# Performance work log

Measured on AMD Instinct MI355X. Metric: run time of the kernel, lower is better.

The kernel has to match this reference:

```python
import jax, jax.numpy as jnp
import numpy as np

B, W, N = 128, 128, 64
HID = 150  # lstm_hid_dim == recon_hid_dim
L = 2      # layer_numb


def _edges_fc(n):
    # for j in range(n) for i in range(n) if i != j -> row0 = i (src), row1 = j (dst)
    a = np.arange(n)
    src = np.concatenate([np.delete(a, j) for j in range(n)])
    dst = np.repeat(a, n - 1)
    return np.stack([src, dst]).astype(np.int32)


def _edges_tc(w):
    # for j in range(w) for i in range(j) -> row0 = i (src), row1 = j (dst)
    src = np.concatenate([np.arange(j) for j in range(1, w)])
    dst = np.repeat(np.arange(w), np.arange(w))
    return np.stack([src, dst]).astype(np.int32)


def _batch_edges(e, b, n):
    # tile per-graph edges b times with node offsets (block-diagonal batched graph)
    off = (jnp.arange(b) * n).astype(e.dtype)
    return (e[:, None, :] + off[None, :, None]).reshape(2, -1)


def _gat_conv(x, edge_index, w, a_src, a_dst, b):
    # PyG GATConv, heads=1: h = x W^T; e_ij = LeakyReLU(a_src.h_j + a_dst.h_i); softmax over dst
    m = x.shape[0]
    loop = jnp.arange(m, dtype=edge_index.dtype)
    src = jnp.concatenate([edge_index[0], loop])
    dst = jnp.concatenate([edge_index[1], loop])
    h = x @ w.T
    e = jax.nn.leaky_relu(h @ a_src, 0.2)[src] + jax.nn.leaky_relu(jnp.zeros((), h.dtype), 0.2) * 0
    e = jax.nn.leaky_relu((h @ a_src)[src] + (h @ a_dst)[dst], 0.2)
    emax = jax.ops.segment_max(e, dst, num_segments=m)
    ex = jnp.exp(e - emax[dst])
    denom = jax.ops.segment_sum(ex, dst, num_segments=m)
    alpha = ex / denom[dst]
    out = jax.ops.segment_sum(h[src] * alpha[:, None], dst, num_segments=m)
    return out + b


def _gcn_conv(x, edge_index, w, b):
    # PyG GCNConv: add self loops, D^{-1/2} A D^{-1/2} (x W^T) + b
    m = x.shape[0]
    loop = jnp.arange(m, dtype=edge_index.dtype)
    src = jnp.concatenate([edge_index[0], loop])
    dst = jnp.concatenate([edge_index[1], loop])
    h = x @ w.T
    deg = jax.ops.segment_sum(jnp.ones(src.shape, h.dtype), dst, num_segments=m)
    dinv = 1.0 / jnp.sqrt(deg)
    norm = dinv[src] * dinv[dst]
    out = jax.ops.segment_sum(h[src] * norm[:, None], dst, num_segments=m)
    return out + b


def _stgat_block(x, fc_e, tc_e, gw, gas, gad, gb, cw, cb):
    x = jax.lax.stop_gradient(x)  # data.clone().detach()
    b, w, n = x.shape
    xp = jnp.transpose(x, (0, 2, 1)).reshape(-1, w)          # [B*N, W]
    f = jax.nn.relu(_gat_conv(xp, fc_e, gw, gas, gad, gb))
    f = f.reshape(b, n, w)
    z = jnp.transpose(f, (0, 2, 1)).reshape(-1, n)           # [B*W, N]
    t = jax.nn.relu(_gcn_conv(z, tc_e, cw, cb))
    t = t.reshape(b, n, w)  # faithful to torch view(B, node_num, -1) quirk
    return jnp.transpose(t, (0, 2, 1))


def _conv_branch(x, w, b, k):
    pad = (k - 1) // 2
    xc = jnp.transpose(x, (0, 2, 1))  # [B, N, W]
    xc = jnp.pad(xc, ((0, 0), (0, 0), (pad, pad)))
    y = jax.lax.conv_general_dilated(xc, w, (1,), 'VALID',
                                     dimension_numbers=('NCH', 'OIH', 'NCH'))
    y = jax.nn.relu(y + b[None, :, None])
    return jnp.transpose(y, (0, 2, 1))


def _lstm_scan(x, w_ih, w_hh, b_ih, b_hh, reverse):
    hdim = w_hh.shape[1]

    def step(carry, xt):
        h, c = carry
        g = xt @ w_ih.T + h @ w_hh.T + b_ih + b_hh
        i, f, gg, o = jnp.split(g, 4, axis=-1)
        c = jax.nn.sigmoid(f) * c + jax.nn.sigmoid(i) * jnp.tanh(gg)
        h = jax.nn.sigmoid(o) * jnp.tanh(c)
        return (h, c), h

    bsz = x.shape[0]
    init = (jnp.zeros((bsz, hdim), x.dtype), jnp.zeros((bsz, hdim), x.dtype))
    xs = jnp.swapaxes(x, 0, 1)  # [T, B, D]
    _, hs = jax.lax.scan(step, init, xs, reverse=reverse)
    return jnp.swapaxes(hs, 0, 1)  # [B, T, H]


def reference(x, fc_edge_index, tc_edge_index,
              conv2_w, conv2_b, conv3_w, conv3_b,
              gat_w, gat_asrc, gat_adst, gat_b, gcn_w, gcn_b,
              lstm_wih, lstm_whh, lstm_bih, lstm_bhh,
              dec_wih, dec_whh, dec_bih, dec_bhh, fc_w, fc_b):
    b, w, n = x.shape
    fc_e = _batch_edges(fc_edge_index, b, n)
    tc_e = _batch_edges(tc_edge_index, b, w)
    hs = [x, _conv_branch(x, conv2_w, conv2_b, 5), _conv_branch(x, conv3_w, conv3_b, 7)]
    nlayers = gat_w.shape[1]
    for t in range(3):
        for l in range(nlayers):
            hs[t] = hs[t] + _stgat_block(hs[t], fc_e, tc_e,
                                         gat_w[t, l], gat_asrc[t, l], gat_adst[t, l],
                                         gat_b[t, l], gcn_w[t, l], gcn_b[t, l])
    h = jnp.concatenate(hs, axis=2)  # [B, W, 3N]
    fwd = _lstm_scan(h, lstm_wih[0], lstm_whh[0], lstm_bih[0], lstm_bhh[0], False)
    bwd = _lstm_scan(h, lstm_wih[1], lstm_whh[1], lstm_bih[1], lstm_bhh[1], True)
    h_end = jnp.concatenate([fwd[:, -1], bwd[:, -1]], axis=-1)  # [B, 2H]
    rep = jnp.repeat(h_end, w, axis=1).reshape(b, w, -1)  # repeat_interleave + view quirk
    dfwd = _lstm_scan(rep, dec_wih[0], dec_whh[0], dec_bih[0], dec_bhh[0], False)
    dbwd = _lstm_scan(rep, dec_wih[1], dec_whh[1], dec_bih[1], dec_bhh[1], True)
    dec = jnp.concatenate([dfwd, dbwd], axis=-1)  # [B, W, 2H]
    return dec @ fc_w.T + fc_b


def setup_inputs() -> dict:
    key = jax.random.key(0)
    ks = jax.random.split(key, 24)
    s = 0.05
    f = lambda k, shp: jax.random.normal(k, shp, jnp.float32) * s
    return {
        'x': jax.random.normal(ks[0], (B, W, N), jnp.float32),
        'fc_edge_index': jnp.asarray(_edges_fc(N)),
        'tc_edge_index': jnp.asarray(_edges_tc(W)),
        'conv2_w': f(ks[1], (N, N, 5)), 'conv2_b': f(ks[2], (N,)),
        'conv3_w': f(ks[3], (N, N, 7)), 'conv3_b': f(ks[4], (N,)),
        'gat_w': f(ks[5], (3, L, W, W)), 'gat_asrc': f(ks[6], (3, L, W)),
        'gat_adst': f(ks[7], (3, L, W)), 'gat_b': f(ks[8], (3, L, W)),
        'gcn_w': f(ks[9], (3, L, N, N)), 'gcn_b': f(ks[10], (3, L, N)),
        'lstm_wih': f(ks[11], (2, 4 * HID, 3 * N)), 'lstm_whh': f(ks[12], (2, 4 * HID, HID)),
        'lstm_bih': f(ks[13], (2, 4 * HID)), 'lstm_bhh': f(ks[14], (2, 4 * HID)),
        'dec_wih': f(ks[15], (2, 4 * HID, 2 * HID)), 'dec_whh': f(ks[16], (2, 4 * HID, HID)),
        'dec_bih': f(ks[17], (2, 4 * HID)), 'dec_bhh': f(ks[18], (2, 4 * HID)),
        'fc_w': f(ks[19], (N, 2 * HID)), 'fc_b': f(ks[20], (N,)),
    }
```

## Files before the change

kernel.cpp:

```cpp
#include <hip/hip_runtime.h>
#include <hip/hip_fp16.h>


typedef _Float16 v2h __attribute__((ext_vector_type(2)));

__device__ __forceinline__ float sigm(float x) {
    return 1.0f / (1.0f + __expf(-x));
}
__device__ __forceinline__ float tanhfast(float x) {
    return 2.0f / (1.0f + __expf(-2.0f * x)) - 1.0f;
}
__device__ __forceinline__ v2h pk2(float a, float b) {
    v2h r; r[0] = (_Float16)a; r[1] = (_Float16)b; return r;
}
__device__ __forceinline__ unsigned pku(float a, float b) {
    return __builtin_bit_cast(unsigned, pk2(a, b));
}
__device__ __forceinline__ v2h upk(unsigned u) { return __builtin_bit_cast(v2h, u); }
__device__ __forceinline__ float fdot2(v2h a, v2h b, float c) {
#if __has_builtin(__builtin_amdgcn_fdot2)
    return __builtin_amdgcn_fdot2(a, b, c, false);
#else
    return c + (float)a[0] * (float)b[0] + (float)a[1] * (float)b[1];
#endif
}

__device__ __forceinline__ void barrier_lds() {
    asm volatile("s_waitcnt lgkmcnt(0)" ::: "memory");
    __builtin_amdgcn_s_barrier();
}

__global__ void k_copy(const float* __restrict__ x, float* __restrict__ hs0) {
    int i = blockIdx.x * 256 + threadIdx.x;
    ((float4*)hs0)[i] = ((const float4*)x)[i];
}

__global__ __launch_bounds__(256) void k_conv2(
    const float* __restrict__ x,
    const float* __restrict__ cw5, const float* __restrict__ cb5,
    const float* __restrict__ cw7, const float* __restrict__ cb7,
    float* __restrict__ hs1, float* __restrict__ hs2) {
    extern __shared__ float S[];
    float* xt = S;
    float* wl = S + 70 * 68;
    int b = blockIdx.x, wh = blockIdx.y, br = blockIdx.z;
    int K = br ? 7 : 5;
    const float* cw = br ? cw7 : cw5;
    const float* cb = br ? cb7 : cb5;
    float* dst = br ? hs2 : hs1;
    int w0 = wh * 64;
    int tid = threadIdx.x;

    for (int f = tid; f < 70 * 64; f += 256) {
        int ww = f >> 6, i = f & 63;
        int wp = w0 - 3 + ww;
        xt[ww * 68 + i] = ((unsigned)wp < 128u) ? x[b * 8192 + wp * 64 + i] : 0.f;
    }
    int nw = K * 4096;
    for (int f = tid; f < nw; f += 256) {
        int j = f & 3, o = (f >> 2) & 63, i4 = (f >> 8) & 15, t = f >> 12;
        wl[f] = cw[(o * 64 + i4 * 4 + j) * K + t];
    }
    __syncthreads();

    int to = tid & 15, tw = tid >> 4;
    float acc[4][4] = {};
    int ob = 3 - (K >> 1);
    for (int t = 0; t < K; ++t) {
        int rbase = tw * 4 + t + ob;
        for (int i4 = 0; i4 < 16; ++i4) {
            float4 a0 = *(const float4*)&xt[(rbase + 0) * 68 + i4 * 4];
            float4 a1 = *(const float4*)&xt[(rbase + 1) * 68 + i4 * 4];
            float4 a2 = *(const float4*)&xt[(rbase + 2) * 68 + i4 * 4];
            float4 a3 = *(const float4*)&xt[(rbase + 3) * 68 + i4 * 4];
            const float* wrow = &wl[(t * 16 + i4) * 256];
            float4 b0 = *(const float4*)&wrow[to * 4];
            float4 b1 = *(const float4*)&wrow[(to + 16) * 4];
            float4 b2 = *(const float4*)&wrow[(to + 32) * 4];
            float4 b3 = *(const float4*)&wrow[(to + 48) * 4];
            #define DOT4(w_, a_) \
                acc[w_][0] = fmaf(a_.x, b0.x, acc[w_][0]); acc[w_][0] = fmaf(a_.y, b0.y, acc[w_][0]); \
                acc[w_][0] = fmaf(a_.z, b0.z, acc[w_][0]); acc[w_][0] = fmaf(a_.w, b0.w, acc[w_][0]); \
                acc[w_][1] = fmaf(a_.x, b1.x, acc[w_][1]); acc[w_][1] = fmaf(a_.y, b1.y, acc[w_][1]); \
                acc[w_][1] = fmaf(a_.z, b1.z, acc[w_][1]); acc[w_][1] = fmaf(a_.w, b1.w, acc[w_][1]); \
                acc[w_][2] = fmaf(a_.x, b2.x, acc[w_][2]); acc[w_][2] = fmaf(a_.y, b2.y, acc[w_][2]); \
                acc[w_][2] = fmaf(a_.z, b2.z, acc[w_][2]); acc[w_][2] = fmaf(a_.w, b2.w, acc[w_][2]); \
                acc[w_][3] = fmaf(a_.x, b3.x, acc[w_][3]); acc[w_][3] = fmaf(a_.y, b3.y, acc[w_][3]); \
                acc[w_][3] = fmaf(a_.z, b3.z, acc[w_][3]); acc[w_][3] = fmaf(a_.w, b3.w, acc[w_][3]);
            DOT4(0, a0)
            DOT4(1, a1)
            DOT4(2, a2)
            DOT4(3, a3)
            #undef DOT4
        }
    }
    #pragma unroll
    for (int wj = 0; wj < 4; ++wj) {
        int w = w0 + tw * 4 + wj;
        #pragma unroll
        for (int oj = 0; oj < 4; ++oj) {
            int o = to + 16 * oj;
            dst[b * 8192 + w * 64 + o] = fmaxf(acc[wj][oj] + cb[o], 0.f);
        }
    }
}

__global__ __launch_bounds__(256, 2) void k_stgat(
    float* __restrict__ hs0, float* __restrict__ hs1, float* __restrict__ hs2,
    const float* __restrict__ gat_w, const float* __restrict__ gat_asrc,
    const float* __restrict__ gat_adst, const float* __restrict__ gat_b,
    const float* __restrict__ gcn_w, const float* __restrict__ gcn_b, int l) {
    extern __shared__ float S[];
    _Float16* Sh = (_Float16*)S;
    const int XHh = 0;
    const int GHh = 8448;
    const int HHTh = 25344;
    const int AHh = 34560;
    const int FHh = 8448;
    const int CHh = 0;
    const int SDo = 17024;
    const int CSo = 17024;
    const int HGo = 8576;

    int b = blockIdx.x, br = blockIdx.y, tid = threadIdx.x;
    float* hs = (br == 0 ? hs0 : (br == 1 ? hs1 : hs2)) + b * 8192;
    int wsel = br * 2 + l;
    const float* gw = gat_w + wsel * 16384;
    const float* asr = gat_asrc + wsel * 128;
    const float* ads = gat_adst + wsel * 128;
    const float* gb = gat_b + wsel * 128;
    const float* cwp = gcn_w + wsel * 4096;
    const float* cbp = gcn_b + wsel * 64;

    {
        const float4* hsv = (const float4*)hs;
        for (int mt = tid; mt < 512; mt += 256) {
            int ng = mt & 15, wg = mt >> 4;
            float4 r0 = hsv[(wg * 4 + 0) * 16 + ng];
            float4 r1 = hsv[(wg * 4 + 1) * 16 + ng];
            float4 r2 = hsv[(wg * 4 + 2) * 16 + ng];
            float4 r3 = hsv[(wg * 4 + 3) * 16 + ng];
            int n0 = ng * 4, ww = wg * 4;
            *(uint2*)&Sh[XHh + (n0 + 0) * 132 + ww] = make_uint2(pku(r0.x, r1.x), pku(r2.x, r3.x));
            *(uint2*)&Sh[XHh + (n0 + 1) * 132 + ww] = make_uint2(pku(r0.y, r1.y), pku(r2.y, r3.y));
            *(uint2*)&Sh[XHh + (n0 + 2) * 132 + ww] = make_uint2(pku(r0.z, r1.z), pku(r2.z, r3.z));
            *(uint2*)&Sh[XHh + (n0 + 3) * 132 + ww] = make_uint2(pku(r0.w, r1.w), pku(r2.w, r3.w));
        }
        const float4* gwv = (const float4*)gw;
        for (int f4 = tid; f4 < 4096; f4 += 256) {
            float4 v = gwv[f4];
            int wo = f4 >> 5, k4 = f4 & 31;
            *(uint2*)&Sh[GHh + wo * 132 + k4 * 4] = make_uint2(pku(v.x, v.y), pku(v.z, v.w));
        }
    }
    __syncthreads();

    int wq = tid & 15, nq = tid >> 4;
    {
        float asv[8], adv[8];
        #pragma unroll
        for (int c = 0; c < 8; ++c) { asv[c] = asr[wq + 16 * c]; adv[c] = ads[wq + 16 * c]; }
        float acc0[8] = {}, acc1[8] = {}, acc2[8] = {}, acc3[8] = {};
        const _Float16* Arow = Sh + XHh + nq * 4 * 132;
        const _Float16* Brow = Sh + GHh + wq * 132;
        for (int k4 = 0; k4 < 32; ++k4) {
            uint2 u0 = *(const uint2*)&Arow[k4 * 4];
            uint2 u1 = *(const uint2*)&Arow[132 + k4 * 4];
            uint2 u2 = *(const uint2*)&Arow[264 + k4 * 4];
            uint2 u3 = *(const uint2*)&Arow[396 + k4 * 4];
            v2h a0l = upk(u0.x), a0h = upk(u0.y), a1l = upk(u1.x), a1h = upk(u1.y);
            v2h a2l = upk(u2.x), a2h = upk(u2.y), a3l = upk(u3.x), a3h = upk(u3.y);
            #pragma unroll
            for (int c = 0; c < 8; ++c) {
                uint2 ub = *(const uint2*)&Brow[c * (16 * 132) + k4 * 4];
                v2h bl = upk(ub.x), bh = upk(ub.y);
                acc0[c] = fdot2(a0l, bl, acc0[c]); acc0[c] = fdot2(a0h, bh, acc0[c]);
                acc1[c] = fdot2(a1l, bl, acc1[c]); acc1[c] = fdot2(a1h, bh, acc1[c]);
                acc2[c] = fdot2(a2l, bl, acc2[c]); acc2[c] = fdot2(a2h, bh, acc2[c]);
                acc3[c] = fdot2(a3l, bl, acc3[c]); acc3[c] = fdot2(a3h, bh, acc3[c]);
            }
        }
        #pragma unroll
        for (int c = 0; c < 8; ++c)
            *(uint2*)&Sh[HHTh + (wq + 16 * c) * 68 + nq * 4] =
                make_uint2(pku(acc0[c], acc1[c]), pku(acc2[c], acc3[c]));
        float ps0 = 0, ps1 = 0, ps2 = 0, ps3 = 0, pd0 = 0, pd1 = 0, pd2 = 0, pd3 = 0;
        #pragma unroll
        for (int c = 0; c < 8; ++c) {
            ps0 = fmaf(acc0[c], asv[c], ps0); ps1 = fmaf(acc1[c], asv[c], ps1);
            ps2 = fmaf(acc2[c], asv[c], ps2); ps3 = fmaf(acc3[c], asv[c], ps3);
            pd0 = fmaf(acc0[c], adv[c], pd0); pd1 = fmaf(acc1[c], adv[c], pd1);
            pd2 = fmaf(acc2[c], adv[c], pd2); pd3 = fmaf(acc3[c], adv[c], pd3);
        }
        #pragma unroll
        for (int m = 1; m < 16; m <<= 1) {
            ps0 += __shfl_xor(ps0, m); ps1 += __shfl_xor(ps1, m);
            ps2 += __shfl_xor(ps2, m); ps3 += __shfl_xor(ps3, m);
            pd0 += __shfl_xor(pd0, m); pd1 += __shfl_xor(pd1, m);
            pd2 += __shfl_xor(pd2, m); pd3 += __shfl_xor(pd3, m);
        }
        if (wq == 0) {
            S[SDo + nq * 4 + 0] = ps0; S[SDo + nq * 4 + 1] = ps1;
            S[SDo + nq * 4 + 2] = ps2; S[SDo + nq * 4 + 3] = ps3;
            S[SDo + 64 + nq * 4 + 0] = pd0; S[SDo + 64 + nq * 4 + 1] = pd1;
            S[SDo + 64 + nq * 4 + 2] = pd2; S[SDo + 64 + nq * 4 + 3] = pd3;
        }
    }
    __syncthreads();

    {
        const float4* cwv = (const float4*)cwp;
        for (int f4 = tid; f4 < 1024; f4 += 256) {
            float4 v = cwv[f4];
            int c = f4 >> 4, k4 = f4 & 15;
            *(uint2*)&Sh[CHh + c * 68 + k4 * 4] = make_uint2(pku(v.x, v.y), pku(v.z, v.w));
        }
        if (tid < 64) {
            int j = tid;
            float dj = S[SDo + 64 + j];
            float mx = -1e30f;
            for (int i = 0; i < 64; ++i) {
                float e = S[SDo + i] + dj;
                e = (e > 0.f) ? e : 0.2f * e;
                mx = fmaxf(mx, e);
            }
            float sum = 0.f;
            for (int i = 0; i < 64; i += 2) {
                float e0 = S[SDo + i] + dj;     e0 = (e0 > 0.f) ? e0 : 0.2f * e0;
                float e1 = S[SDo + i + 1] + dj; e1 = (e1 > 0.f) ? e1 : 0.2f * e1;
                float x0 = __expf(e0 - mx), x1 = __expf(e1 - mx);
                sum += x0 + x1;
                *(unsigned*)&Sh[AHh + j * 68 + i] = pku(x0, x1);
            }
            float rinv = 1.f / sum;
            for (int i = 0; i < 64; i += 2) {
                v2h v = upk(*(const unsigned*)&Sh[AHh + j * 68 + i]);
                *(unsigned*)&Sh[AHh + j * 68 + i] = pku((float)v[0] * rinv, (float)v[1] * rinv);
            }
        }
    }
    __syncthreads();

    {
        float gbv[8];
        #pragma unroll
        for (int c = 0; c < 8; ++c) gbv[c] = gb[wq + 16 * c];
        float acc0[8] = {}, acc1[8] = {}, acc2[8] = {}, acc3[8] = {};
        const _Float16* Arow = Sh + AHh + nq * 4 * 68;
        const _Float16* Brow = Sh + HHTh + wq * 68;
        for (int k4 = 0; k4 < 16; ++k4) {
            uint2 u0 = *(const uint2*)&Arow[k4 * 4];
            uint2 u1 = *(const uint2*)&Arow[68 + k4 * 4];
            uint2 u2 = *(const uint2*)&Arow[136 + k4 * 4];
            uint2 u3 = *(const uint2*)&Arow[204 + k4 * 4];
            v2h a0l = upk(u0.x), a0h = upk(u0.y), a1l = upk(u1.x), a1h = upk(u1.y);
            v2h a2l = upk(u2.x), a2h = upk(u2.y), a3l = upk(u3.x), a3h = upk(u3.y);
            #pragma unroll
            for (int c = 0; c < 8; ++c) {
                uint2 ub = *(const uint2*)&Brow[c * (16 * 68) + k4 * 4];
                v2h bl = upk(ub.x), bh = upk(ub.y);
                acc0[c] = fdot2(a0l, bl, acc0[c]); acc0[c] = fdot2(a0h, bh, acc0[c]);
                acc1[c] = fdot2(a1l, bl, acc1[c]); acc1[c] = fdot2(a1h, bh, acc1[c]);
                acc2[c] = fdot2(a2l, bl, acc2[c]); acc2[c] = fdot2(a2h, bh, acc2[c]);
                acc3[c] = fdot2(a3l, bl, acc3[c]); acc3[c] = fdot2(a3h, bh, acc3[c]);
            }
        }
        #pragma unroll
        for (int c = 0; c < 8; ++c) {
            float f0 = fmaxf(acc0[c] + gbv[c], 0.f);
            float f1 = fmaxf(acc1[c] + gbv[c], 0.f);
            float f2 = fmaxf(acc2[c] + gbv[c], 0.f);
            float f3 = fmaxf(acc3[c] + gbv[c], 0.f);
            *(uint2*)&Sh[FHh + (wq + 16 * c) * 68 + nq * 4] = make_uint2(pku(f0, f1), pku(f2, f3));
        }
    }
    __syncthreads();

    {
        int cq = tid & 7, wg = tid >> 3;
        float acc0[8] = {}, acc1[8] = {}, acc2[8] = {}, acc3[8] = {};
        const _Float16* Arow = Sh + FHh + wg * 4 * 68;
        const _Float16* Brow = Sh + CHh + cq * 68;
        for (int k4 = 0; k4 < 16; ++k4) {
            uint2 u0 = *(const uint2*)&Arow[k4 * 4];
            uint2 u1 = *(const uint2*)&Arow[68 + k4 * 4];
            uint2 u2 = *(const uint2*)&Arow[136 + k4 * 4];
            uint2 u3 = *(const uint2*)&Arow[204 + k4 * 4];
            v2h a0l = upk(u0.x), a0h = upk(u0.y), a1l = upk(u1.x), a1h = upk(u1.y);
            v2h a2l = upk(u2.x), a2h = upk(u2.y), a3l = upk(u3.x), a3h = upk(u3.y);
            #pragma unroll
            for (int cc = 0; cc < 8; ++cc) {
                uint2 ub = *(const uint2*)&Brow[cc * (8 * 68) + k4 * 4];
                v2h bl = upk(ub.x), bh = upk(ub.y);
                acc0[cc] = fdot2(a0l, bl, acc0[cc]); acc0[cc] = fdot2(a0h, bh, acc0[cc]);
                acc1[cc] = fdot2(a1l, bl, acc1[cc]); acc1[cc] = fdot2(a1h, bh, acc1[cc]);
                acc2[cc] = fdot2(a2l, bl, acc2[cc]); acc2[cc] = fdot2(a2h, bh, acc2[cc]);
                acc3[cc] = fdot2(a3l, bl, acc3[cc]); acc3[cc] = fdot2(a3h, bh, acc3[cc]);
            }
        }
        #pragma unroll
        for (int cc = 0; cc < 8; ++cc) {
            int c = cq + 8 * cc;
            S[HGo + (wg * 4 + 0) * 66 + c] = acc0[cc];
            S[HGo + (wg * 4 + 1) * 66 + c] = acc1[cc];
            S[HGo + (wg * 4 + 2) * 66 + c] = acc2[cc];
            S[HGo + (wg * 4 + 3) * 66 + c] = acc3[cc];
        }
    }
    __syncthreads();

    {
        int c = tid & 63, q = tid >> 6;
        float local = 0.f;
        for (int i = 0; i < 32; ++i) {
            int w = q * 32 + i;
            local = fmaf(rsqrtf((float)(w + 1)), S[HGo + w * 66 + c], local);
        }
        S[CSo + q * 64 + c] = local;
    }
    __syncthreads();
    {
        int c = tid & 63, q = tid >> 6;
        float run = 0.f;
        for (int qq = 0; qq < q; ++qq) run += S[CSo + qq * 64 + c];
        float cbv = cbp[c];
        for (int i = 0; i < 32; ++i) {
            int w = q * 32 + i;
            float dv = rsqrtf((float)(w + 1));
            run = fmaf(dv, S[HGo + w * 66 + c], run);
            S[HGo + w * 66 + c] = fmaxf(fmaf(dv, run, cbv), 0.f);
        }
    }
    __syncthreads();

    {
        float4* hsv4 = (float4*)hs;
        for (int f4 = tid; f4 < 2048; f4 += 256) {
            int a = f4 >> 4, cc0 = (f4 & 15) * 4;
            float4 old = hsv4[f4];
            int n = a & 63, ahi = a >> 6;
            old.x += S[HGo + (cc0 * 2 + ahi) * 66 + n];
            old.y += S[HGo + ((cc0 + 1) * 2 + ahi) * 66 + n];
            old.z += S[HGo + ((cc0 + 2) * 2 + ahi) * 66 + n];
            old.w += S[HGo + ((cc0 + 3) * 2 + ahi) * 66 + n];
            hsv4[f4] = old;
        }
    }
}

__global__ __launch_bounds__(256) void k_encgemm(
    const float* __restrict__ hs0, const float* __restrict__ hs1, const float* __restrict__ hs2,
    const float* __restrict__ wih, const float* __restrict__ bih, const float* __restrict__ bhh,
    float* __restrict__ gx0) {
    __shared__ __align__(16) float At[32 * 132];
    __shared__ __align__(16) float Bt[32 * 68];
    int b = blockIdx.x, ny = blockIdx.y, tid = threadIdx.x;
    int g0 = ny * 64;
    int ty = tid >> 4, tx = tid & 15;
    float acc[8][4];
    #pragma unroll
    for (int r = 0; r < 8; ++r)
        #pragma unroll
        for (int c = 0; c < 4; ++c) acc[r][c] = 0.f;
    const float* hsb[3] = {hs0 + b * 8192, hs1 + b * 8192, hs2 + b * 8192};
    for (int kc = 0; kc < 6; ++kc) {
        const float* src = hsb[kc >> 1] + (kc & 1) * 32;
        for (int f = tid; f < 4096; f += 256) {
            int t = f >> 5, kk = f & 31;
            At[kk * 132 + t] = src[t * 64 + kk];
        }
        for (int f = tid; f < 2048; f += 256) {
            int gg = f >> 5, kk = f & 31;
            int g = g0 + gg;
            Bt[kk * 68 + gg] = (g < 600) ? wih[g * 192 + kc * 32 + kk] : 0.f;
        }
        __syncthreads();
        #pragma unroll 8
        for (int kk = 0; kk < 32; ++kk) {
            float a[8], bb[4];
            *(float4*)&a[0] = *(const float4*)&At[kk * 132 + ty * 8];
            *(float4*)&a[4] = *(const float4*)&At[kk * 132 + ty * 8 + 4];
            *(float4*)&bb[0] = *(const float4*)&Bt[kk * 68 + tx * 4];
            #pragma unroll
            for (int r = 0; r < 8; ++r)
                #pragma unroll
                for (int c = 0; c < 4; ++c) acc[r][c] = fmaf(a[r], bb[c], acc[r][c]);
        }
        __syncthreads();
    }
    for (int r = 0; r < 8; ++r) {
        int t = ty * 8 + r;
        for (int c = 0; c < 4; ++c) {
            int g = g0 + tx * 4 + c;
            if (g < 600) gx0[(b * 128 + t) * 600 + g] = acc[r][c] + bih[g] + bhh[g];
        }
    }
}

__global__ void k_encgx1(const float* __restrict__ hs0, const float* __restrict__ hs1,
                         const float* __restrict__ hs2, const float* __restrict__ wih,
                         const float* __restrict__ bih, const float* __restrict__ bhh,
                         float* __restrict__ gx1) {
    __shared__ __align__(16) float sh[192];
    int b = blockIdx.x, tid = threadIdx.x;
    if (tid < 192) {
        const float* src = (tid < 64 ? hs0 : (tid < 128 ? hs1 : hs2));
        sh[tid] = src[b * 8192 + 127 * 64 + (tid & 63)];
    }
    __syncthreads();
    const float* w1 = wih + 600 * 192;
    for (int g = tid; g < 600; g += 256) {
        float acc = bih[600 + g] + bhh[600 + g];
        const float4* wr = (const float4*)(w1 + g * 192);
        #pragma unroll 8
        for (int q = 0; q < 48; ++q) {
            float4 wv = wr[q];
            float4 hv = *(const float4*)&sh[q * 4];
            acc = fmaf(wv.x, hv.x, acc);
            acc = fmaf(wv.y, hv.y, acc);
            acc = fmaf(wv.z, hv.z, acc);
            acc = fmaf(wv.w, hv.w, acc);
        }
        gx1[b * 600 + g] = acc;
    }
}

__global__ void k_ptpref(const float* __restrict__ dwih, float* __restrict__ PT) {
    int dg = blockIdx.x * 256 + threadIdx.x;
    if (dg >= 1200) return;
    const float* wr = dwih + dg * 300;
    float run = 0.f;
    PT[dg] = 0.f;
    for (int k = 0; k < 300; ++k) {
        run += wr[k];
        PT[(k + 1) * 1200 + dg] = run;
    }
}

__global__ void k_pd(const float* __restrict__ PT, float* __restrict__ PD) {
    int id = blockIdx.x * 256 + threadIdx.x;
    if (id >= 153600) return;
    int g = id % 600;
    int tt = id / 600;
    int t = tt & 127, dir = tt >> 7;
    int dg = dir * 600 + g;
    int base = t * 300;
    int j0 = base >> 7;
    int ke1 = (j0 + 1) * 128 - base;
    int ke2 = ke1 + 128; ke2 = ke2 > 300 ? 300 : ke2;
    int ke3 = ke1 + 256; ke3 = ke3 > 300 ? 300 : ke3;
    float p1 = PT[ke1 * 1200 + dg];
    float p2 = PT[ke2 * 1200 + dg];
    float p3 = PT[ke3 * 1200 + dg];
    float p4 = PT[300 * 1200 + dg];
    float4 o = {p1, p2 - p1, p3 - p2, p4 - p3};
    *(float4*)&PD[id * 4] = o;
}

__global__ __launch_bounds__(640, 3) void k_enclstm(
    const float* __restrict__ gx0, const float* __restrict__ gx1,
    const float* __restrict__ whh, float* __restrict__ h_end) {
    int bid = blockIdx.x, t = threadIdx.x;
    if (bid >= 128) {
        int b = bid - 128;
        if (t < 150) {
            float ai = gx1[b * 600 + t];
            float ag = gx1[b * 600 + 300 + t];
            float ao = gx1[b * 600 + 450 + t];
            float c = sigm(ai) * tanhfast(ag);
            h_end[b * 300 + 150 + t] = sigm(ao) * tanhfast(c);
        }
        return;
    }
    __shared__ __align__(16) _Float16 hbuf[2][152];
    int b = bid;
    bool on = t < 600;
    int j = t >> 2, g4 = t & 3;
    int grow = g4 * 150 + j;
    v2h wv[76];
    #pragma unroll
    for (int p = 0; p < 76; ++p) wv[p] = pk2(0.f, 0.f);
    if (on) {
        const float* r = whh + grow * 150;
        #pragma unroll
        for (int p = 0; p < 75; ++p) wv[p] = pk2(r[2 * p], r[2 * p + 1]);
    }
    for (int i = t; i < 304; i += 640) ((_Float16*)hbuf)[i] = (_Float16)0.f;
    float c = 0.f;
    float xc = on ? gx0[(b * 128) * 600 + grow] : 0.f;
    barrier_lds();
    for (int s = 0; s < 128; ++s) {
        float xn = (on && s < 127) ? gx0[(b * 128 + s + 1) * 600 + grow] : 0.f;
        float s0 = 0.f, s1 = 0.f, s2 = 0.f, s3 = 0.f;
        const float4* hp = (const float4*)hbuf[s & 1];
        #pragma unroll
        for (int cc = 0; cc < 19; ++cc) {
            float4 hv = hp[cc];
            s0 = fdot2(wv[4 * cc + 0], __builtin_bit_cast(v2h, hv.x), s0);
            s1 = fdot2(wv[4 * cc + 1], __builtin_bit_cast(v2h, hv.y), s1);
            s2 = fdot2(wv[4 * cc + 2], __builtin_bit_cast(v2h, hv.z), s2);
            s3 = fdot2(wv[4 * cc + 3], __builtin_bit_cast(v2h, hv.w), s3);
        }
        float a = xc + ((s0 + s1) + (s2 + s3));
        bool isg = (g4 == 2);
        float sg = sigm(isg ? 2.f * a : a);
        float act = isg ? fmaf(2.f, sg, -1.f) : sg;
        float vf = __shfl_xor(act, 1);
        float vg = __shfl_xor(act, 2);
        float vo = __shfl_xor(vf, 2);
        if (on && g4 == 0) {
            c = fmaf(vf, c, act * vg);
            float h = vo * tanhfast(c);
            hbuf[(s + 1) & 1][j] = (_Float16)h;
            if (s == 127) h_end[b * 300 + j] = h;
        }
        xc = xn;
        barrier_lds();
    }
}

__global__ __launch_bounds__(640, 3) void k_declstm(
    const float* __restrict__ PD, const float* __restrict__ hend,
    const float* __restrict__ whh_all, const float* __restrict__ bih,
    const float* __restrict__ bhh, float* __restrict__ dec_out) {
    __shared__ __align__(16) float she[304];
    __shared__ __align__(16) _Float16 hbuf[2][152];
    int dir = blockIdx.x >> 7, b = blockIdx.x & 127;
    int t = threadIdx.x;
    bool on = t < 600;
    int j = t >> 2, g4 = t & 3;
    int grow = g4 * 150 + j;
    v2h wv[76];
    #pragma unroll
    for (int p = 0; p < 76; ++p) wv[p] = pk2(0.f, 0.f);
    float bias = 0.f;
    if (on) {
        const float* r = whh_all + dir * 90000 + grow * 150;
        #pragma unroll
        for (int p = 0; p < 75; ++p) wv[p] = pk2(r[2 * p], r[2 * p + 1]);
        bias = bih[dir * 600 + grow] + bhh[dir * 600 + grow];
    }
    for (int i = t; i < 304; i += 640) she[i] = (i < 300) ? hend[b * 300 + i] : 0.f;
    for (int i = t; i < 304; i += 640) ((_Float16*)hbuf)[i] = (_Float16)0.f;
    float c = 0.f;
    int t0 = dir ? 127 : 0;
    float4 pd = {0.f, 0.f, 0.f, 0.f};
    if (on) pd = *(const float4*)&PD[((dir * 128 + t0) * 600 + grow) * 4];
    barrier_lds();
    for (int s = 0; s < 128; ++s) {
        int tt = dir ? (127 - s) : s;
        float4 pdn = {0.f, 0.f, 0.f, 0.f};
        if (on && s < 127) {
            int tn = dir ? (126 - s) : (s + 1);
            pdn = *(const float4*)&PD[((dir * 128 + tn) * 600 + grow) * 4];
        }
        int j0 = (tt * 300) >> 7;
        float e0 = she[j0], e1 = she[j0 + 1], e2 = she[j0 + 2], e3 = she[j0 + 3];
        float a = bias + e0 * pd.x + e1 * pd.y + e2 * pd.z + e3 * pd.w;
        float s0 = 0.f, s1 = 0.f, s2 = 0.f, s3 = 0.f;
        const float4* hp = (const float4*)hbuf[s & 1];
        #pragma unroll
        for (int cc = 0; cc < 19; ++cc) {
            float4 hv = hp[cc];
            s0 = fdot2(wv[4 * cc + 0], __builtin_bit_cast(v2h, hv.x), s0);
            s1 = fdot2(wv[4 * cc + 1], __builtin_bit_cast(v2h, hv.y), s1);
            s2 = fdot2(wv[4 * cc + 2], __builtin_bit_cast(v2h, hv.z), s2);
            s3 = fdot2(wv[4 * cc + 3], __builtin_bit_cast(v2h, hv.w), s3);
        }
        a += (s0 + s1) + (s2 + s3);
        bool isg = (g4 == 2);
        float sg = sigm(isg ? 2.f * a : a);
        float act = isg ? fmaf(2.f, sg, -1.f) : sg;
        float vf = __shfl_xor(act, 1);
        float vg = __shfl_xor(act, 2);
        float vo = __shfl_xor(vf, 2);
        if (on && g4 == 0) {
            c = fmaf(vf, c, act * vg);
            float h = vo * tanhfast(c);
            hbuf[(s + 1) & 1][j] = (_Float16)h;
            dec_out[(b * 128 + tt) * 300 + dir * 150 + j] = h;
        }
        pd = pdn;
        barrier_lds();
    }
}

__global__ __launch_bounds__(256) void k_fingemm(const float* __restrict__ dec,
                                                 const float* __restrict__ fw,
                                                 const float* __restrict__ fb,
                                                 float* __restrict__ out) {
    __shared__ __align__(16) float AsT[32 * 68];
    __shared__ __align__(16) float FwT[32 * 68];
    int r0 = blockIdx.x * 64, tid = threadIdx.x;
    int ty = tid >> 4, tx = tid & 15;
    float acc[4][4];
    #pragma unroll
    for (int r = 0; r < 4; ++r)
        #pragma unroll
        for (int c = 0; c < 4; ++c) acc[r][c] = 0.f;
    for (int kc = 0; kc < 10; ++kc) {
        int k0 = kc * 32;
        for (int f = tid; f < 2048; f += 256) {
            int m = f >> 5, kk = f & 31;
            int k = k0 + kk;
            AsT[kk * 68 + m] = (k < 300) ? dec[(r0 + m) * 300 + k] : 0.f;
        }
        for (int f = tid; f < 2048; f += 256) {
            int n = f >> 5, kk = f & 31;
            int k = k0 + kk;
            FwT[kk * 68 + n] = (k < 300) ? fw[n * 300 + k] : 0.f;
        }
        __syncthreads();
        #pragma unroll 8
        for (int kk = 0; kk < 32; ++kk) {
            float a[4], w[4];
            *(float4*)&a[0] = *(const float4*)&AsT[kk * 68 + ty * 4];
            *(float4*)&w[0] = *(const float4*)&FwT[kk * 68 + tx * 4];
            #pragma unroll
            for (int r = 0; r < 4; ++r)
                #pragma unroll
                for (int c = 0; c < 4; ++c) acc[r][c] = fmaf(a[r], w[c], acc[r][c]);
        }
        __syncthreads();
    }
    for (int r = 0; r < 4; ++r) {
        int m = r0 + ty * 4 + r;
        float4 o4;
        o4.x = acc[r][0] + fb[tx * 4 + 0];
        o4.y = acc[r][1] + fb[tx * 4 + 1];
        o4.z = acc[r][2] + fb[tx * 4 + 2];
        o4.w = acc[r][3] + fb[tx * 4 + 3];
        *(float4*)&out[m * 64 + tx * 4] = o4;
    }
}

extern "C" void kernel_launch(void* const* d_in, const int* in_sizes, int n_in,
                              void* d_out, int out_size, void* d_ws, size_t ws_size,
                              hipStream_t stream) {
    const float* x = (const float*)d_in[0];
    const float* c2w = (const float*)d_in[3];
    const float* c2b = (const float*)d_in[4];
    const float* c3w = (const float*)d_in[5];
    const float* c3b = (const float*)d_in[6];
    const float* gatw = (const float*)d_in[7];
    const float* gatas = (const float*)d_in[8];
    const float* gatad = (const float*)d_in[9];
    const float* gatb = (const float*)d_in[10];
    const float* gcnw = (const float*)d_in[11];
    const float* gcnb = (const float*)d_in[12];
    const float* lwih = (const float*)d_in[13];
    const float* lwhh = (const float*)d_in[14];
    const float* lbih = (const float*)d_in[15];
    const float* lbhh = (const float*)d_in[16];
    const float* dwih = (const float*)d_in[17];
    const float* dwhh = (const float*)d_in[18];
    const float* dbih = (const float*)d_in[19];
    const float* dbhh = (const float*)d_in[20];
    const float* fcw = (const float*)d_in[21];
    const float* fcb = (const float*)d_in[22];
    float* out = (float*)d_out;
    float* ws = (float*)d_ws;

    float* hs0 = ws;
    float* hs1 = ws + 1048576;
    float* hs2 = ws + 2097152;
    float* gx0 = ws + 3145728;
    float* gx1 = ws + 12976128;
    float* hend = ws + 13052928;
    float* PT = ws + 13091328;
    float* dec = ws + 13452528;
    float* PD = hs0;

    k_copy<<<1024, 256, 0, stream>>>(x, hs0);
    k_conv2<<<dim3(128, 2, 2), 256, (70 * 68 + 7 * 16 * 256) * 4, stream>>>(
        x, c2w, c2b, c3w, c3b, hs1, hs2);
    for (int l = 0; l < 2; ++l)
        k_stgat<<<dim3(128, 3), 256, 77824, stream>>>(hs0, hs1, hs2, gatw, gatas,
                                                      gatad, gatb, gcnw, gcnb, l);
    k_encgemm<<<dim3(128, 10), 256, 0, stream>>>(hs0, hs1, hs2, lwih, lbih, lbhh, gx0);
    k_encgx1<<<128, 256, 0, stream>>>(hs0, hs1, hs2, lwih, lbih, lbhh, gx1);
    k_ptpref<<<5, 256, 0, stream>>>(dwih, PT);
    k_pd<<<600, 256, 0, stream>>>(PT, PD);
    k_enclstm<<<256, 640, 0, stream>>>(gx0, gx1, lwhh, hend);
    k_declstm<<<256, 640, 0, stream>>>(PD, hend, dwhh, dbih, dbhh, dec);
    k_fingemm<<<256, 256, 0, stream>>>(dec, fcw, fcb, out);
}
```

Before: 569.3 us.

## Use fp16 packed dot products in encoder input GEMM and final FC GEMM

The encoder input-projection GEMM is rewritten to stage fp16 copies of activations and weights in XOR-swizzled shared memory, using 128x128 tiles and fdot2 accumulation in fp32. The decoder LSTM now writes its outputs as fp16, and the final FC GEMM reads these half values and uses packed fdot2, halving its loads and global traffic. The aim is to cut FMA instruction count and memory bandwidth in the two GEMMs, at the cost of fp16 rounding of inputs and decoder outputs.

```diff
diff --git a/kernel.cpp b/kernel.cpp
--- a/kernel.cpp
+++ b/kernel.cpp
@@ -348,51 +348,83 @@
     }
 }
 
-__global__ __launch_bounds__(256) void k_encgemm(
+__global__ __launch_bounds__(256) void k_encgemm2(
     const float* __restrict__ hs0, const float* __restrict__ hs1, const float* __restrict__ hs2,
     const float* __restrict__ wih, const float* __restrict__ bih, const float* __restrict__ bhh,
     float* __restrict__ gx0) {
-    __shared__ __align__(16) float At[32 * 132];
-    __shared__ __align__(16) float Bt[32 * 68];
-    int b = blockIdx.x, ny = blockIdx.y, tid = threadIdx.x;
-    int g0 = ny * 64;
+    __shared__ __align__(16) _Float16 Xh[128 * 72];
+    __shared__ __align__(16) _Float16 Wh[128 * 72];
+    int b = blockIdx.x, gy = blockIdx.y, tid = threadIdx.x;
+    int g0 = gy * 128;
     int ty = tid >> 4, tx = tid & 15;
-    float acc[8][4];
+    float acc[8][8];
     #pragma unroll
-    for (int r = 0; r < 8; ++r)
-        #pragma unroll
-        for (int c = 0; c < 4; ++c) acc[r][c] = 0.f;
+    for (int i = 0; i < 8; ++i)
+        #pragma unroll
+        for (int j = 0; j < 8; ++j) acc[i][j] = 0.f;
     const float* hsb[3] = {hs0 + b * 8192, hs1 + b * 8192, hs2 + b * 8192};
-    for (int kc = 0; kc < 6; ++kc) {
-        const float* src = hsb[kc >> 1] + (kc & 1) * 32;
-        for (int f = tid; f < 4096; f += 256) {
-            int t = f >> 5, kk = f & 31;
-            At[kk * 132 + t] = src[t * 64 + kk];
-        }
+
+    for (int c = 0; c < 3; ++c) {
+        const float4* src = (const float4*)hsb[c];
         for (int f = tid; f < 2048; f += 256) {
-            int gg = f >> 5, kk = f & 31;
-            int g = g0 + gg;
-            Bt[kk * 68 + gg] = (g < 600) ? wih[g * 192 + kc * 32 + kk] : 0.f;
+            int t = f >> 4, k4 = f & 15;
+            float4 v = src[f];
+            int pos = (((k4 >> 1) ^ ((t >> 3) & 7)) << 1) + (k4 & 1);
+            *(uint2*)&Xh[t * 72 + pos * 4] = make_uint2(pku(v.x, v.y), pku(v.z, v.w));
+        }
+        for (int f = tid; f < 2048; f += 256) {
+            int g = f >> 4, k4 = f & 15;
+            int gg = g0 + g;
+            float4 v = (gg < 600) ? *(const float4*)&wih[gg * 192 + c * 64 + k4 * 4]
+                                  : make_float4(0.f, 0.f, 0.f, 0.f);
+            int pos = (((k4 >> 1) ^ ((g >> 3) & 7)) << 1) + (k4 & 1);
+            *(uint2*)&Wh[g * 72 + pos * 4] = make_uint2(pku(v.x, v.y), pku(v.z, v.w));
         }
         __syncthreads();
-        #pragma unroll 8
-        for (int kk = 0; kk < 32; ++kk) {
-            float a[8], bb[4];
-            *(float4*)&a[0] = *(const float4*)&At[kk * 132 + ty * 8];
-            *(float4*)&a[4] = *(const float4*)&At[kk * 132 + ty * 8 + 4];
-            *(float4*)&bb[0] = *(const float4*)&Bt[kk * 68 + tx * 4];
+        #pragma unroll
+        for (int k8 = 0; k8 < 8; ++k8) {
+            uint4 av[8];
             #pragma unroll
-            for (int r = 0; r < 8; ++r)
+            for (int i = 0; i < 8; ++i) {
+                int row = ty * 8 + i;
+                av[i] = *(const uint4*)&Xh[row * 72 + (k8 ^ ((row >> 3) & 7)) * 8];
+            }
+            #pragma unroll
+            for (int j = 0; j < 8; ++j) {
+                int row = tx * 8 + j;
+                uint4 bv = *(const uint4*)&Wh[row * 72 + (k8 ^ ((row >> 3) & 7)) * 8];
+                v2h b0 = upk(bv.x), b1 = upk(bv.y), b2 = upk(bv.z), b3 = upk(bv.w);
                 #pragma unroll
-                for (int c = 0; c < 4; ++c) acc[r][c] = fmaf(a[r], bb[c], acc[r][c]);
+                for (int i = 0; i < 8; ++i) {
+                    acc[i][j] = fdot2(upk(av[i].x), b0, acc[i][j]);
+                    acc[i][j] = fdot2(upk(av[i].y), b1, acc[i][j]);
+                    acc[i][j] = fdot2(upk(av[i].z), b2, acc[i][j]);
+                    acc[i][j] = fdot2(upk(av[i].w), b3, acc[i][j]);
+                }
+            }
         }
         __syncthreads();
     }
-    for (int r = 0; r < 8; ++r) {
-        int t = ty * 8 + r;
-        for (int c = 0; c < 4; ++c) {
-            int g = g0 + tx * 4 + c;
-            if (g < 600) gx0[(b * 128 + t) * 600 + g] = acc[r][c] + bih[g] + bhh[g];
+    #pragma unroll
+    for (int i = 0; i < 8; ++i) {
+        int t = ty * 8 + i;
+        float* orow = gx0 + (b * 128 + t) * 600;
+        #pragma unroll
+        for (int jj = 0; jj < 2; ++jj) {
+            int gbase = g0 + tx * 8 + jj * 4;
+            if (gbase + 3 < 600) {
+                float4 o;
+                o.x = acc[i][jj * 4 + 0] + bih[gbase + 0] + bhh[gbase + 0];
+                o.y = acc[i][jj * 4 + 1] + bih[gbase + 1] + bhh[gbase + 1];
+                o.z = acc[i][jj * 4 + 2] + bih[gbase + 2] + bhh[gbase + 2];
+                o.w = acc[i][jj * 4 + 3] + bih[gbase + 3] + bhh[gbase + 3];
+                *(float4*)&orow[gbase] = o;
+            } else {
+                for (int e = 0; e < 4; ++e) {
+                    int g = gbase + e;
+                    if (g < 600) orow[g] = acc[i][jj * 4 + e] + bih[g] + bhh[g];
+                }
+            }
         }
     }
 }
@@ -522,7 +554,7 @@
 __global__ __launch_bounds__(640, 3) void k_declstm(
     const float* __restrict__ PD, const float* __restrict__ hend,
     const float* __restrict__ whh_all, const float* __restrict__ bih,
-    const float* __restrict__ bhh, float* __restrict__ dec_out) {
+    const float* __restrict__ bhh, _Float16* __restrict__ dec_out) {
     __shared__ __align__(16) float she[304];
     __shared__ __align__(16) _Float16 hbuf[2][152];
     int dir = blockIdx.x >> 7, b = blockIdx.x & 127;
@@ -578,19 +610,19 @@
             c = fmaf(vf, c, act * vg);
             float h = vo * tanhfast(c);
             hbuf[(s + 1) & 1][j] = (_Float16)h;
-            dec_out[(b * 128 + tt) * 300 + dir * 150 + j] = h;
+            dec_out[(b * 128 + tt) * 300 + dir * 150 + j] = (_Float16)h;
         }
         pd = pdn;
         barrier_lds();
     }
 }
 
-__global__ __launch_bounds__(256) void k_fingemm(const float* __restrict__ dec,
+__global__ __launch_bounds__(256) void k_fingemm(const _Float16* __restrict__ decH,
                                                  const float* __restrict__ fw,
                                                  const float* __restrict__ fb,
                                                  float* __restrict__ out) {
-    __shared__ __align__(16) float AsT[32 * 68];
-    __shared__ __align__(16) float FwT[32 * 68];
+    __shared__ __align__(16) unsigned AsT[16 * 68];
+    __shared__ __align__(16) unsigned FwT[16 * 68];
     int r0 = blockIdx.x * 64, tid = threadIdx.x;
     int ty = tid >> 4, tx = tid & 15;
     float acc[4][4];
@@ -600,26 +632,33 @@
         for (int c = 0; c < 4; ++c) acc[r][c] = 0.f;
     for (int kc = 0; kc < 10; ++kc) {
         int k0 = kc * 32;
-        for (int f = tid; f < 2048; f += 256) {
-            int m = f >> 5, kk = f & 31;
-            int k = k0 + kk;
-            AsT[kk * 68 + m] = (k < 300) ? dec[(r0 + m) * 300 + k] : 0.f;
-        }
-        for (int f = tid; f < 2048; f += 256) {
-            int n = f >> 5, kk = f & 31;
-            int k = k0 + kk;
-            FwT[kk * 68 + n] = (k < 300) ? fw[n * 300 + k] : 0.f;
+        for (int f = tid; f < 1024; f += 256) {
+            int m = f >> 4, kk2 = f & 15;
+            int k = k0 + kk2 * 2;
+            AsT[kk2 * 68 + m] =
+                (k + 1 < 300) ? *(const unsigned*)&decH[(r0 + m) * 300 + k] : 0u;
+        }
+        for (int f = tid; f < 1024; f += 256) {
+            int n = f >> 4, kk2 = f & 15;
+            int k = k0 + kk2 * 2;
+            FwT[kk2 * 68 + n] =
+                (k + 1 < 300) ? pku(fw[n * 300 + k], fw[n * 300 + k + 1]) : 0u;
         }
         __syncthreads();
-        #pragma unroll 8
-        for (int kk = 0; kk < 32; ++kk) {
-            float a[4], w[4];
-            *(float4*)&a[0] = *(const float4*)&AsT[kk * 68 + ty * 4];
-            *(float4*)&w[0] = *(const float4*)&FwT[kk * 68 + tx * 4];
-            #pragma unroll
-            for (int r = 0; r < 4; ++r)
-                #pragma unroll
-                for (int c = 0; c < 4; ++c) acc[r][c] = fmaf(a[r], w[c], acc[r][c]);
+        #pragma unroll 4
+        for (int kk2 = 0; kk2 < 16; ++kk2) {
+            uint4 a4 = *(const uint4*)&AsT[kk2 * 68 + ty * 4];
+            uint4 w4 = *(const uint4*)&FwT[kk2 * 68 + tx * 4];
+            v2h a0 = upk(a4.x), a1 = upk(a4.y), a2 = upk(a4.z), a3 = upk(a4.w);
+            v2h w0 = upk(w4.x), w1 = upk(w4.y), w2 = upk(w4.z), w3 = upk(w4.w);
+            acc[0][0] = fdot2(a0, w0, acc[0][0]); acc[0][1] = fdot2(a0, w1, acc[0][1]);
+            acc[0][2] = fdot2(a0, w2, acc[0][2]); acc[0][3] = fdot2(a0, w3, acc[0][3]);
+            acc[1][0] = fdot2(a1, w0, acc[1][0]); acc[1][1] = fdot2(a1, w1, acc[1][1]);
+            acc[1][2] = fdot2(a1, w2, acc[1][2]); acc[1][3] = fdot2(a1, w3, acc[1][3]);
+            acc[2][0] = fdot2(a2, w0, acc[2][0]); acc[2][1] = fdot2(a2, w1, acc[2][1]);
+            acc[2][2] = fdot2(a2, w2, acc[2][2]); acc[2][3] = fdot2(a2, w3, acc[2][3]);
+            acc[3][0] = fdot2(a3, w0, acc[3][0]); acc[3][1] = fdot2(a3, w1, acc[3][1]);
+            acc[3][2] = fdot2(a3, w2, acc[3][2]); acc[3][3] = fdot2(a3, w3, acc[3][3]);
         }
         __syncthreads();
     }
@@ -668,7 +707,7 @@
     float* gx1 = ws + 12976128;
     float* hend = ws + 13052928;
     float* PT = ws + 13091328;
-    float* dec = ws + 13452528;
+    _Float16* decH = (_Float16*)(ws + 13452528);
     float* PD = hs0;
 
     k_copy<<<1024, 256, 0, stream>>>(x, hs0);
@@ -677,11 +716,11 @@
     for (int l = 0; l < 2; ++l)
         k_stgat<<<dim3(128, 3), 256, 77824, stream>>>(hs0, hs1, hs2, gatw, gatas,
                                                       gatad, gatb, gcnw, gcnb, l);
-    k_encgemm<<<dim3(128, 10), 256, 0, stream>>>(hs0, hs1, hs2, lwih, lbih, lbhh, gx0);
+    k_encgemm2<<<dim3(128, 5), 256, 0, stream>>>(hs0, hs1, hs2, lwih, lbih, lbhh, gx0);
     k_encgx1<<<128, 256, 0, stream>>>(hs0, hs1, hs2, lwih, lbih, lbhh, gx1);
     k_ptpref<<<5, 256, 0, stream>>>(dwih, PT);
     k_pd<<<600, 256, 0, stream>>>(PT, PD);
     k_enclstm<<<256, 640, 0, stream>>>(gx0, gx1, lwhh, hend);
-    k_declstm<<<256, 640, 0, stream>>>(PD, hend, dwhh, dbih, dbhh, dec);
-    k_fingemm<<<256, 256, 0, stream>>>(dec, fcw, fcb, out);
-}
+    k_declstm<<<256, 640, 0, stream>>>(PD, hend, dwhh, dbih, dbhh, decH);
+    k_fingemm<<<256, 256, 0, stream>>>(decH, fcw, fcb, out);
+}
```

Result: faster. 543.0 us, median of 2 (-4.6%).
